# Kernel tuning notes

Hardware: AMD Instinct MI355X
Metric: run time of the kernel (lower is better)

The kernel has to match this reference:

```python
import jax, jax.numpy as jnp
import numpy as np

N_NODES = 50000
N_EDGES = 800000
HC = 64      # hidden_channels
NG = 5       # num_gaussians
NF = 64      # num_filters
SL = 20      # short_len
NC = 2       # n_conv
Z_DIM = 2 * NF + SL  # 148
BN_EPS = 1e-5


def setup_inputs() -> dict:
    key = jax.random.key(0)
    ks = jax.random.split(key, 16)
    s = 0.05
    return {
        "h": jax.random.normal(ks[0], (N_NODES, HC), dtype=jnp.float32),
        "edge_index": jax.random.randint(ks[1], (2, N_EDGES), 0, N_NODES, dtype=jnp.int32),
        "edge_weight": jax.random.uniform(ks[2], (N_EDGES,), dtype=jnp.float32),
        "edge_attr": jax.random.uniform(ks[3], (N_EDGES, NG), dtype=jnp.float32),
        "lin0_w": jax.random.normal(ks[4], (HC, NF), dtype=jnp.float32) * s,
        "lin0_b": jnp.zeros((NF,), dtype=jnp.float32),
        "short_w": jax.random.normal(ks[5], (NG, SL), dtype=jnp.float32) * s,
        "short_b": jnp.zeros((SL,), dtype=jnp.float32),
        "linf_w": jax.random.normal(ks[6], (NC, Z_DIM, NF), dtype=jnp.float32) * s,
        "linf_b": jnp.zeros((NC, NF), dtype=jnp.float32),
        "lins_w": jax.random.normal(ks[7], (NC, Z_DIM, NF), dtype=jnp.float32) * s,
        "lins_b": jnp.zeros((NC, NF), dtype=jnp.float32),
        "bn_gamma": jnp.ones((NC, NF), dtype=jnp.float32),
        "bn_beta": jnp.zeros((NC, NF), dtype=jnp.float32),
        "data": 0,
    }


def reference(h, edge_index, edge_weight, edge_attr,
              lin0_w, lin0_b, short_w, short_b,
              linf_w, linf_b, lins_w, lins_b,
              bn_gamma, bn_beta, data):
    # lin0 + relu
    out = jax.nn.relu(h @ lin0_w + lin0_b)                      # [N, NF]
    # short edge-attr projection + relu
    ea = jax.nn.relu(edge_attr @ short_w + short_b)             # [E, SL]
    src = edge_index[0]  # x_j (source)
    dst = edge_index[1]  # x_i (target / aggregation index)
    n = out.shape[0]
    for l in range(NC):
        x_i = out[dst]                                          # [E, NF]
        x_j = out[src]                                          # [E, NF]
        z = jnp.concatenate([x_i, x_j, ea], axis=-1)            # [E, 148]
        msg = jax.nn.sigmoid(z @ linf_w[l] + linf_b[l]) * \
              jax.nn.softplus(z @ lins_w[l] + lins_b[l])        # [E, NF]
        agg = jax.ops.segment_sum(msg, dst, num_segments=n)     # [N, NF]
        # BatchNorm1d (training-mode batch stats, biased variance)
        mean = jnp.mean(agg, axis=0)
        var = jnp.mean((agg - mean) ** 2, axis=0)
        bn = (agg - mean) * jax.lax.rsqrt(var + BN_EPS) * bn_gamma[l] + bn_beta[l]
        conv_out = bn + out                                     # CGConv internal residual
        out = out + jax.nn.relu(conv_out)                       # _Interactions residual
    return out
```

## Files before the change

### kernel.cpp

```cpp
#include <hip/hip_runtime.h>
#include <hip/hip_bf16.h>

#define N_NODES 50000
#define N_EDGES 800000
#define SCAN_NB 49
#define EPW 20
#define EW_BLOCKS 10000

typedef __hip_bfloat16 bf16;
typedef unsigned int u32;
typedef unsigned short u16;
typedef _Float16 hh2 __attribute__((ext_vector_type(2)));

#if defined(__has_builtin)
#if __has_builtin(__builtin_amdgcn_fdot2)
#define HAVE_FDOT2 1
#endif
#endif

__device__ __forceinline__ float bfb(u32 b) { return __uint_as_float(b << 16); }

__device__ __forceinline__ u16 f2bf(float x) {
    bf16 a = __float2bfloat16(x);
    u16 u;
    __builtin_memcpy(&u, &a, 2);
    return u;
}

__device__ __forceinline__ hh2 pkrtz(float a, float b) {
    auto r = __builtin_amdgcn_cvt_pkrtz(a, b);
    hh2 o;
    __builtin_memcpy(&o, &r, 4);
    return o;
}

__device__ __forceinline__ float ldf(const void* p, long i, int f32) {
    if (f32) return ((const float*)p)[i];
    return bfb((u32)((const u16*)p)[i]);
}

__device__ __forceinline__ int detect_f32(const u32* g) { return g[0] == 0x3F800000u; }

__global__ __launch_bounds__(256) void k_front(const void* __restrict__ h,
        const void* __restrict__ w, const void* __restrict__ b,
        const u32* __restrict__ gr, u16* __restrict__ outw,
        const int* __restrict__ ei, int* __restrict__ cnt,
        int* __restrict__ tsum, uint4* __restrict__ aggz4,
        const void* __restrict__ eattr, const void* __restrict__ short_w,
        const void* __restrict__ short_b, u32* __restrict__ sea_e) {
    int t = threadIdx.x;
    uint4 z4 = {0u, 0u, 0u, 0u};
    for (int i = blockIdx.x * 256 + t; i < N_NODES * 16; i += 1536 * 256)
        aggz4[i] = z4;
    int f32 = detect_f32(gr);
    if (blockIdx.x >= 1024) {
        __shared__ float swl[100];
        __shared__ float sbl[20];
        if (t < 100) swl[t] = ldf(short_w, t, f32);
        if (t < 20) sbl[t] = ldf(short_b, t, f32);
        __syncthreads();
        int bid = blockIdx.x - 1024;
        for (int e = bid * 256 + t; e < N_EDGES; e += 512 * 256) {
            float a0 = ldf(eattr, (long)e * 5 + 0, f32);
            float a1 = ldf(eattr, (long)e * 5 + 1, f32);
            float a2 = ldf(eattr, (long)e * 5 + 2, f32);
            float a3 = ldf(eattr, (long)e * 5 + 3, f32);
            float a4 = ldf(eattr, (long)e * 5 + 4, f32);
            u32 buf[10];
            #pragma unroll
            for (int j = 0; j < 10; ++j) {
                float e0 = sbl[2 * j], e1 = sbl[2 * j + 1];
                e0 = fmaf(a0, swl[0 * 20 + 2 * j], e0);
                e1 = fmaf(a0, swl[0 * 20 + 2 * j + 1], e1);
                e0 = fmaf(a1, swl[1 * 20 + 2 * j], e0);
                e1 = fmaf(a1, swl[1 * 20 + 2 * j + 1], e1);
                e0 = fmaf(a2, swl[2 * 20 + 2 * j], e0);
                e1 = fmaf(a2, swl[2 * 20 + 2 * j + 1], e1);
                e0 = fmaf(a3, swl[3 * 20 + 2 * j], e0);
                e1 = fmaf(a3, swl[3 * 20 + 2 * j + 1], e1);
                e0 = fmaf(a4, swl[4 * 20 + 2 * j], e0);
                e1 = fmaf(a4, swl[4 * 20 + 2 * j + 1], e1);
                e0 = fmaxf(e0, 0.f);
                e1 = fmaxf(e1, 0.f);
                hh2 h2 = pkrtz(e0, e1);
                u32 u;
                __builtin_memcpy(&u, &h2, 4);
                buf[j] = u;
            }
            u32* sp = sea_e + (size_t)e * 10u;
            #pragma unroll
            for (int q = 0; q < 5; ++q) {
                uint2 v2 = {buf[2 * q], buf[2 * q + 1]};
                *(uint2*)(sp + 2 * q) = v2;
            }
        }
        return;
    }
    if (blockIdx.x >= 512) {
        __shared__ int lts[SCAN_NB];
        if (t < SCAN_NB) lts[t] = 0;
        __syncthreads();
        int bid = blockIdx.x - 512;
        for (int e = bid * 256 + t; e < N_EDGES; e += 512 * 256) {
            int dst = ei[N_EDGES + e];
            atomicAdd(&cnt[dst], 1);
            atomicAdd(&lts[dst >> 10], 1);
        }
        __syncthreads();
        if (t < SCAN_NB) atomicAdd(&tsum[t], lts[t]);
        return;
    }
    __shared__ float Wl[64 * 64];
    __shared__ float bl[64];
    __shared__ float hs[16 * 64];
    for (int i = t; i < 4096; i += 256) Wl[i] = ldf(w, i, f32);
    if (t < 64) bl[t] = ldf(b, t, f32);
    int c = t & 63, g = t >> 6;
    for (int chunk = blockIdx.x; chunk < N_NODES / 16; chunk += 512) {
        __syncthreads();
        int node0 = chunk * 16;
        for (int i = t; i < 1024; i += 256) hs[i] = ldf(h, (long)node0 * 64 + i, f32);
        __syncthreads();
        #pragma unroll
        for (int nn = 0; nn < 4; ++nn) {
            int n = g * 4 + nn;
            float acc = bl[c];
            #pragma unroll
            for (int k = 0; k < 64; ++k) acc = fmaf(hs[n * 64 + k], Wl[k * 64 + c], acc);
            outw[(node0 + n) * 64 + c] = f2bf(fmaxf(acc, 0.f));
        }
    }
}

__global__ __launch_bounds__(1024) void k_scan(int* __restrict__ cnt,
        const int* __restrict__ tsum) {
    __shared__ int wsum[16];
    __shared__ int boff_s;
    int t = threadIdx.x, lane = t & 63, wv = t >> 6;
    if (wv == 0) {
        int v = (lane < SCAN_NB && lane < (int)blockIdx.x) ? tsum[lane] : 0;
        #pragma unroll
        for (int d = 32; d >= 1; d >>= 1) v += __shfl_xor(v, d, 64);
        if (lane == 0) boff_s = v;
    }
    int i = blockIdx.x * 1024 + t;
    int v = (i < N_NODES) ? cnt[i] : 0;
    int incl = v;
    #pragma unroll
    for (int d = 1; d < 64; d <<= 1) {
        int x = __shfl_up(incl, d, 64);
        if (lane >= d) incl += x;
    }
    if (lane == 63) wsum[wv] = incl;
    __syncthreads();
    if (wv == 0) {
        int s = (lane < 16) ? wsum[lane] : 0;
        int si = s;
        #pragma unroll
        for (int d = 1; d < 16; d <<= 1) {
            int x = __shfl_up(si, d, 64);
            if (lane >= d) si += x;
        }
        if (lane < 16) wsum[lane] = si - s;
    }
    __syncthreads();
    incl += wsum[wv] + boff_s;
    if (i < N_NODES) cnt[i] = incl - v;
}

__global__ __launch_bounds__(256) void k_pproj_bin(const u16* __restrict__ outw,
        const void* __restrict__ linf_w, const void* __restrict__ lins_w,
        const void* __restrict__ linf_b, const void* __restrict__ lins_b,
        const u32* __restrict__ gr, bf16* __restrict__ P,
        const int* __restrict__ ei, int* __restrict__ cursor,
        uint2* __restrict__ bb, u32* __restrict__ wpk) {
    int t = threadIdx.x;
    int f32 = detect_f32(gr);
    if (blockIdx.x >= 512) {
        if (blockIdx.x == 512 && t < 128) {
            int ly = t >> 6, ln = t & 63;
            long wb = (long)ly * 9472 + 8192;
            u32* wp = wpk + (size_t)(ly * 64 + ln) * 20;
            #pragma unroll
            for (int j = 0; j < 10; ++j) {
                hh2 fp = pkrtz(ldf(linf_w, wb + (2 * j) * 64 + ln, f32),
                               ldf(linf_w, wb + (2 * j + 1) * 64 + ln, f32));
                hh2 sp = pkrtz(ldf(lins_w, wb + (2 * j) * 64 + ln, f32),
                               ldf(lins_w, wb + (2 * j + 1) * 64 + ln, f32));
                u32 uf, us;
                __builtin_memcpy(&uf, &fp, 4);
                __builtin_memcpy(&us, &sp, 4);
                wp[2 * j] = uf;
                wp[2 * j + 1] = us;
            }
        }
        int bid = blockIdx.x - 512;
        for (int e = bid * 256 + t; e < N_EDGES; e += 512 * 256) {
            int dst = ei[N_EDGES + e];
            int src = ei[e];
            int slot = atomicAdd(&cursor[dst], 1);
            uint2 v;
            v.x = ((u32)dst << 16) | (u32)src;
            v.y = (u32)e;
            bb[slot] = v;
        }
        return;
    }
    int b = t >> 6, c = t & 63;
    const void* wmat = (b < 2) ? linf_w : lins_w;
    long woff = (long)(b & 1) * 4096;
    float bias = 0.f;
    if (b == 0) bias = ldf(linf_b, c, f32);
    if (b == 2) bias = ldf(lins_b, c, f32);
    float wc[64];
    #pragma unroll
    for (int k = 0; k < 64; ++k) wc[k] = ldf(wmat, woff + k * 64 + c, f32);
    int stidx = (b & 1) * 128 + 2 * c + (b >> 1);
    __shared__ float hs[16 * 64];
    for (int chunk = blockIdx.x; chunk < N_NODES / 16; chunk += 512) {
        __syncthreads();
        int node0 = chunk * 16;
        {
            ushort4 hv = *(const ushort4*)(outw + (size_t)node0 * 64 + t * 4);
            hs[t * 4 + 0] = bfb((u32)hv.x);
            hs[t * 4 + 1] = bfb((u32)hv.y);
            hs[t * 4 + 2] = bfb((u32)hv.z);
            hs[t * 4 + 3] = bfb((u32)hv.w);
        }
        __syncthreads();
        for (int n = 0; n < 16; ++n) {
            float acc = bias;
            #pragma unroll
            for (int k = 0; k < 64; ++k) acc = fmaf(hs[n * 64 + k], wc[k], acc);
            P[(size_t)(node0 + n) * 256 + stidx] = __float2bfloat16(acc);
        }
    }
}

struct EB { u32 ea; u32 pd[4]; u32 ps[4]; int d[4]; };

__global__ __launch_bounds__(256) void k_edge_flat(const uint2* __restrict__ bb,
        const u32* __restrict__ sea_e, const u32* __restrict__ wpk, int layer,
        const u32* __restrict__ Pw, float* __restrict__ agg) {
    int t = threadIdx.x, lane = t & 63, wv = t >> 6;
    int wid = blockIdx.x * 4 + wv;
    int base = wid * EPW;

    int eo = (lane / 10) & 3, j10 = lane % 10;
    const uint4* wv4 = (const uint4*)(wpk + (size_t)(layer * 64 + lane) * 20);
    uint4 q0 = wv4[0], q1 = wv4[1], q2 = wv4[2], q3 = wv4[3], q4 = wv4[4];
    u32 wbuf[20] = {q0.x, q0.y, q0.z, q0.w, q1.x, q1.y, q1.z, q1.w,
                    q2.x, q2.y, q2.z, q2.w, q3.x, q3.y, q3.z, q3.w,
                    q4.x, q4.y, q4.z, q4.w};
    hh2 wf2[10], ws2[10];
    #pragma unroll
    for (int j = 0; j < 10; ++j) {
        __builtin_memcpy(&wf2[j], &wbuf[2 * j], 4);
        __builtin_memcpy(&ws2[j], &wbuf[2 * j + 1], 4);
    }

    float acc = 0.f;
    int cur = -1;

    auto issueA = [&](uint2& A, int b) {
        A = bb[(u32)base + 4u * (u32)b + ((u32)lane & 3u)];
    };
    auto issueB = [&](EB& B, uint2 A, int b) {
        u32 eid = (u32)__shfl((int)A.y, eo, 64);
        B.ea = sea_e[eid * 10u + (u32)j10];
        #pragma unroll
        for (int i = 0; i < 4; ++i) {
            u32 pki = (u32)__builtin_amdgcn_readlane((int)A.x, i);
            int d = (int)(pki >> 16);
            u32 s = pki & 0xFFFFu;
            B.d[i] = d;
            B.pd[i] = Pw[(u32)d * 128u + (u32)lane];
            B.ps[i] = Pw[s * 128u + 64u + (u32)lane];
        }
    };
    auto computeC = [&](const EB& B) {
        #pragma unroll
        for (int i = 0; i < 4; ++i) {
            int d = B.d[i];
            u32 pd = B.pd[i], ps = B.ps[i];
            float f = bfb(pd & 0xFFFFu) + bfb(ps & 0xFFFFu);
            float s = __uint_as_float(pd & 0xFFFF0000u) +
                      __uint_as_float(ps & 0xFFFF0000u);
            #pragma unroll
            for (int j = 0; j < 10; ++j) {
                u32 u = (u32)__builtin_amdgcn_readlane((int)B.ea, 10 * i + j);
                hh2 hu;
                __builtin_memcpy(&hu, &u, 4);
#ifdef HAVE_FDOT2
                f = __builtin_amdgcn_fdot2(hu, wf2[j], f, false);
                s = __builtin_amdgcn_fdot2(hu, ws2[j], s, false);
#else
                f = fmaf((float)hu[0], (float)wf2[j][0], f);
                f = fmaf((float)hu[1], (float)wf2[j][1], f);
                s = fmaf((float)hu[0], (float)ws2[j][0], s);
                s = fmaf((float)hu[1], (float)ws2[j][1], s);
#endif
            }
            float sig = 1.f / (1.f + __expf(-f));
            float sp = fmaxf(s, 0.f) + __logf(1.f + __expf(-fabsf(s)));
            if (d != cur) {
                if (cur >= 0)
                    atomicAdd(agg + (u32)cur * 64u + (u32)lane, acc);
                acc = 0.f;
                cur = d;
            }
            acc += sig * sp;
        }
    };

    uint2 A0, A1, A2, A3;
    EB B0, B1, B2, B3;
    issueA(A0, 0); issueA(A1, 1); issueA(A2, 2); issueA(A3, 3);
    issueB(B0, A0, 0); issueB(B1, A1, 1); issueB(B2, A2, 2);
    issueA(A0, 4);
    issueB(B3, A3, 3);
    computeC(B0);
    issueB(B0, A0, 4);
    computeC(B1);
    computeC(B2);
    computeC(B3);
    computeC(B0);
    if (cur >= 0) atomicAdd(agg + (u32)cur * 64u + (u32)lane, acc);
}

__global__ __launch_bounds__(256) void k_stats(const float* __restrict__ aggf,
        float* __restrict__ stats) {
    int t = threadIdx.x;
    int r = t >> 4, c4 = (t & 15) * 4;
    float s0 = 0.f, s1 = 0.f, s2 = 0.f, s3 = 0.f;
    float q0 = 0.f, q1 = 0.f, q2 = 0.f, q3 = 0.f;
    for (int row = blockIdx.x * 16 + r; row < N_NODES; row += 256 * 16) {
        float4 v = *(const float4*)(aggf + (size_t)row * 64 + c4);
        s0 += v.x; s1 += v.y; s2 += v.z; s3 += v.w;
        q0 = fmaf(v.x, v.x, q0); q1 = fmaf(v.y, v.y, q1);
        q2 = fmaf(v.z, v.z, q2); q3 = fmaf(v.w, v.w, q3);
    }
    __shared__ float red[2][16][64];
    red[0][r][c4 + 0] = s0; red[0][r][c4 + 1] = s1;
    red[0][r][c4 + 2] = s2; red[0][r][c4 + 3] = s3;
    red[1][r][c4 + 0] = q0; red[1][r][c4 + 1] = q1;
    red[1][r][c4 + 2] = q2; red[1][r][c4 + 3] = q3;
    __syncthreads();
    if (t < 128) {
        int m = t >> 6, c = t & 63;
        float a = 0.f;
        #pragma unroll
        for (int k = 0; k < 16; ++k) a += red[m][k][c];
        atomicAdd(&stats[m * 64 + c], a);
    }
}

__global__ __launch_bounds__(256) void k_apply_pproj(float* __restrict__ aggf,
        const float* __restrict__ stats, const void* __restrict__ gamma,
        const void* __restrict__ beta, const u32* __restrict__ gr,
        u16* __restrict__ outw,
        const void* __restrict__ linf_w, const void* __restrict__ lins_w,
        const void* __restrict__ linf_b, const void* __restrict__ lins_b,
        bf16* __restrict__ P) {
    int f32 = detect_f32(gr);
    int t = threadIdx.x;
    int b = t >> 6, c = t & 63;
    int nid = t >> 4, c4 = (t & 15) * 4;
    const float invN = 1.f / (float)N_NODES;
    float m4[4], iv4[4], g4[4], b4[4];
    #pragma unroll
    for (int k = 0; k < 4; ++k) {
        float mean = stats[c4 + k] * invN;
        float var = fmaxf(stats[64 + c4 + k] * invN - mean * mean, 0.f);
        m4[k] = mean;
        iv4[k] = rsqrtf(var + 1e-5f);
        g4[k] = ldf(gamma, c4 + k, f32);
        b4[k] = ldf(beta, c4 + k, f32);
    }
    const void* wmat = (b < 2) ? linf_w : lins_w;
    long woff = 9472 + (long)(b & 1) * 4096;
    float bias = 0.f;
    if (b == 0) bias = ldf(linf_b, 64 + c, f32);
    if (b == 2) bias = ldf(lins_b, 64 + c, f32);
    float wc[64];
    #pragma unroll
    for (int k = 0; k < 64; ++k) wc[k] = ldf(wmat, woff + k * 64 + c, f32);
    int stidx = (b & 1) * 128 + 2 * c + (b >> 1);
    __shared__ float hs[16 * 64];
    for (int chunk = blockIdx.x; chunk < N_NODES / 16; chunk += 512) {
        __syncthreads();
        int node0 = chunk * 16;
        {
            size_t idx = (size_t)(node0 + nid) * 64 + c4;
            float4 a = *(const float4*)(aggf + idx);
            ushort4 ow = *(const ushort4*)(outw + idx);
            const float* ap = (const float*)&a;
            const u16* op = (const u16*)&ow;
            float no[4];
            #pragma unroll
            for (int k = 0; k < 4; ++k) {
                float o = bfb((u32)op[k]);
                float bn = fmaf((ap[k] - m4[k]) * iv4[k], g4[k], b4[k]);
                no[k] = o + fmaxf(bn + o, 0.f);
            }
            ushort4 nw = {f2bf(no[0]), f2bf(no[1]), f2bf(no[2]), f2bf(no[3])};
            *(ushort4*)(outw + idx) = nw;
            float4 z4 = {0.f, 0.f, 0.f, 0.f};
            *(float4*)(aggf + idx) = z4;
            float4 hv = {no[0], no[1], no[2], no[3]};
            *(float4*)(&hs[nid * 64 + c4]) = hv;
        }
        __syncthreads();
        for (int n = 0; n < 16; ++n) {
            float acc = bias;
            #pragma unroll
            for (int k = 0; k < 64; ++k) acc = fmaf(hs[n * 64 + k], wc[k], acc);
            P[(size_t)(node0 + n) * 256 + stidx] = __float2bfloat16(acc);
        }
    }
}

__global__ __launch_bounds__(256) void k_apply_final(const float* __restrict__ aggf,
        const float* __restrict__ stats, const void* __restrict__ gamma,
        const void* __restrict__ beta, const u32* __restrict__ gr,
        const u16* __restrict__ outw, void* __restrict__ dout) {
    int f32 = detect_f32(gr);
    const float invN = 1.f / (float)N_NODES;
    int t0 = blockIdx.x * 256 + threadIdx.x;
    int c4 = (t0 & 15) * 4;
    float m4[4], iv4[4], g4[4], b4[4];
    #pragma unroll
    for (int k = 0; k < 4; ++k) {
        float mean = stats[c4 + k] * invN;
        float var = fmaxf(stats[64 + c4 + k] * invN - mean * mean, 0.f);
        m4[k] = mean;
        iv4[k] = rsqrtf(var + 1e-5f);
        g4[k] = ldf(gamma, 64 + c4 + k, f32);
        b4[k] = ldf(beta, 64 + c4 + k, f32);
    }
    for (int i4 = t0; i4 < N_NODES * 16; i4 += 1024 * 256) {
        float4 a = *(const float4*)(aggf + (size_t)i4 * 4);
        ushort4 ow = *(const ushort4*)(outw + (size_t)i4 * 4);
        const float* ap = (const float*)&a;
        const u16* op = (const u16*)&ow;
        float no[4];
        #pragma unroll
        for (int k = 0; k < 4; ++k) {
            float o = bfb((u32)op[k]);
            float bn = fmaf((ap[k] - m4[k]) * iv4[k], g4[k], b4[k]);
            no[k] = o + fmaxf(bn + o, 0.f);
        }
        if (f32) {
            float4 o4 = {no[0], no[1], no[2], no[3]};
            *(float4*)((float*)dout + (size_t)i4 * 4) = o4;
        } else {
            ushort4 o4 = {f2bf(no[0]), f2bf(no[1]), f2bf(no[2]), f2bf(no[3])};
            *(ushort4*)((u16*)dout + (size_t)i4 * 4) = o4;
        }
    }
}

extern "C" void kernel_launch(void* const* d_in, const int* in_sizes, int n_in,
                              void* d_out, int out_size, void* d_ws, size_t ws_size,
                              hipStream_t stream) {
    const void* h       = d_in[0];
    const int*  ei      = (const int*)d_in[1];
    const void* eattr   = d_in[3];
    const void* lin0_w  = d_in[4];
    const void* lin0_b  = d_in[5];
    const void* short_w = d_in[6];
    const void* short_b = d_in[7];
    const void* linf_w  = d_in[8];
    const void* linf_b  = d_in[9];
    const void* lins_w  = d_in[10];
    const void* lins_b  = d_in[11];
    const void* gamma   = d_in[12];
    const void* beta    = d_in[13];
    const u32*  gr      = (const u32*)gamma;

    u16*   outw  = (u16*)d_ws;
    bf16*  P     = (bf16*)(outw + (size_t)N_NODES * 64);
    uint2* bb    = (uint2*)(P + (size_t)N_NODES * 256);
    float* aggf  = (float*)(bb + N_EDGES);
    int*   cnt   = (int*)(aggf + (size_t)N_NODES * 64);
    float* stats = (float*)(cnt + N_NODES);
    int*   tsum  = (int*)(stats + 256);
    u32*   sea_e = (u32*)(tsum + 64);
    u32*   wpk   = sea_e + (size_t)N_EDGES * 10;

    size_t zbytes = (size_t)N_NODES * 4 + 256 * 4 + 64 * 4;
    (void)hipMemsetAsync(cnt, 0, zbytes, stream);

    k_front<<<1536, 256, 0, stream>>>(h, lin0_w, lin0_b, gr, outw, ei, cnt,
                                      tsum, (uint4*)aggf, eattr, short_w,
                                      short_b, sea_e);
    k_scan<<<SCAN_NB, 1024, 0, stream>>>(cnt, tsum);
    k_pproj_bin<<<1024, 256, 0, stream>>>(outw, linf_w, lins_w, linf_b, lins_b,
                                          gr, P, ei, cnt, bb, wpk);
    k_edge_flat<<<EW_BLOCKS, 256, 0, stream>>>(bb, sea_e, wpk, 0,
                                               (const u32*)P, aggf);
    k_stats<<<256, 256, 0, stream>>>(aggf, stats);
    k_apply_pproj<<<512, 256, 0, stream>>>(aggf, stats, gamma, beta, gr, outw,
                                           linf_w, lins_w, linf_b, lins_b, P);
    k_edge_flat<<<EW_BLOCKS, 256, 0, stream>>>(bb, sea_e, wpk, 1,
                                               (const u32*)P, aggf);
    k_stats<<<256, 256, 0, stream>>>(aggf, stats + 128);
    k_apply_final<<<1024, 256, 0, stream>>>(aggf, stats + 128, gamma, beta, gr,
                                            outw, d_out);
}
```

Baseline: 459.7 us.

## Replace global-atomic counting sort with two-pass bucketed radix binning of edges

```diff
diff --git a/kernel.cpp b/kernel.cpp
--- a/kernel.cpp
+++ b/kernel.cpp
@@ -3,7 +3,7 @@
 
 #define N_NODES 50000
 #define N_EDGES 800000
-#define SCAN_NB 49
+#define NBK 391
 #define EPW 20
 #define EW_BLOCKS 10000
 
@@ -44,8 +44,8 @@
 __global__ __launch_bounds__(256) void k_front(const void* __restrict__ h,
         const void* __restrict__ w, const void* __restrict__ b,
         const u32* __restrict__ gr, u16* __restrict__ outw,
-        const int* __restrict__ ei, int* __restrict__ cnt,
-        int* __restrict__ tsum, uint4* __restrict__ aggz4,
+        const int* __restrict__ ei, u32* __restrict__ bmat,
+        uint4* __restrict__ aggz4,
         const void* __restrict__ eattr, const void* __restrict__ short_w,
         const void* __restrict__ short_b, u32* __restrict__ sea_e) {
     int t = threadIdx.x;
@@ -97,17 +97,17 @@
         return;
     }
     if (blockIdx.x >= 512) {
-        __shared__ int lts[SCAN_NB];
-        if (t < SCAN_NB) lts[t] = 0;
+        __shared__ int bcnt[NBK];
+        for (int k = t; k < NBK; k += 256) bcnt[k] = 0;
         __syncthreads();
         int bid = blockIdx.x - 512;
         for (int e = bid * 256 + t; e < N_EDGES; e += 512 * 256) {
             int dst = ei[N_EDGES + e];
-            atomicAdd(&cnt[dst], 1);
-            atomicAdd(&lts[dst >> 10], 1);
-        }
-        __syncthreads();
-        if (t < SCAN_NB) atomicAdd(&tsum[t], lts[t]);
+            atomicAdd(&bcnt[dst >> 7], 1);
+        }
+        __syncthreads();
+        for (int k = t; k < NBK; k += 256)
+            bmat[(size_t)k * 512 + bid] = (u32)bcnt[k];
         return;
     }
     __shared__ float Wl[64 * 64];
@@ -132,19 +132,12 @@
     }
 }
 
-__global__ __launch_bounds__(1024) void k_scan(int* __restrict__ cnt,
-        const int* __restrict__ tsum) {
-    __shared__ int wsum[16];
-    __shared__ int boff_s;
+__global__ __launch_bounds__(512) void k_scan(u32* __restrict__ bmat,
+        u32* __restrict__ total) {
+    __shared__ int wsum[8];
     int t = threadIdx.x, lane = t & 63, wv = t >> 6;
-    if (wv == 0) {
-        int v = (lane < SCAN_NB && lane < (int)blockIdx.x) ? tsum[lane] : 0;
-        #pragma unroll
-        for (int d = 32; d >= 1; d >>= 1) v += __shfl_xor(v, d, 64);
-        if (lane == 0) boff_s = v;
-    }
-    int i = blockIdx.x * 1024 + t;
-    int v = (i < N_NODES) ? cnt[i] : 0;
+    int bk = blockIdx.x;
+    int v = (int)bmat[(size_t)bk * 512 + t];
     int incl = v;
     #pragma unroll
     for (int d = 1; d < 64; d <<= 1) {
@@ -154,26 +147,56 @@
     if (lane == 63) wsum[wv] = incl;
     __syncthreads();
     if (wv == 0) {
-        int s = (lane < 16) ? wsum[lane] : 0;
+        int s = (lane < 8) ? wsum[lane] : 0;
         int si = s;
         #pragma unroll
-        for (int d = 1; d < 16; d <<= 1) {
+        for (int d = 1; d < 8; d <<= 1) {
             int x = __shfl_up(si, d, 64);
             if (lane >= d) si += x;
         }
-        if (lane < 16) wsum[lane] = si - s;
-    }
-    __syncthreads();
-    incl += wsum[wv] + boff_s;
-    if (i < N_NODES) cnt[i] = incl - v;
+        if (lane < 8) wsum[lane] = si - s;
+    }
+    __syncthreads();
+    int excl = incl - v + wsum[wv];
+    bmat[(size_t)bk * 512 + t] = (u32)excl;
+    if (t == 511) total[bk] = (u32)(excl + v);
+}
+
+__global__ __launch_bounds__(512) void k_scan2(const u32* __restrict__ total,
+        u32* __restrict__ bucketbase) {
+    __shared__ int wsum[8];
+    int t = threadIdx.x, lane = t & 63, wv = t >> 6;
+    int v = (t < NBK) ? (int)total[t] : 0;
+    int incl = v;
+    #pragma unroll
+    for (int d = 1; d < 64; d <<= 1) {
+        int x = __shfl_up(incl, d, 64);
+        if (lane >= d) incl += x;
+    }
+    if (lane == 63) wsum[wv] = incl;
+    __syncthreads();
+    if (wv == 0) {
+        int s = (lane < 8) ? wsum[lane] : 0;
+        int si = s;
+        #pragma unroll
+        for (int d = 1; d < 8; d <<= 1) {
+            int x = __shfl_up(si, d, 64);
+            if (lane >= d) si += x;
+        }
+        if (lane < 8) wsum[lane] = si - s;
+    }
+    __syncthreads();
+    if (t < NBK) bucketbase[t] = (u32)(incl - v + wsum[wv]);
+    if (t == 0) bucketbase[NBK] = N_EDGES;
 }
 
 __global__ __launch_bounds__(256) void k_pproj_bin(const u16* __restrict__ outw,
         const void* __restrict__ linf_w, const void* __restrict__ lins_w,
         const void* __restrict__ linf_b, const void* __restrict__ lins_b,
         const u32* __restrict__ gr, bf16* __restrict__ P,
-        const int* __restrict__ ei, int* __restrict__ cursor,
-        uint2* __restrict__ bb, u32* __restrict__ wpk) {
+        const int* __restrict__ ei, const u32* __restrict__ bmat,
+        const u32* __restrict__ bucketbase, uint2* __restrict__ tmp,
+        u32* __restrict__ wpk) {
     int t = threadIdx.x;
     int f32 = detect_f32(gr);
     if (blockIdx.x >= 512) {
@@ -194,15 +217,19 @@
                 wp[2 * j + 1] = us;
             }
         }
+        __shared__ u32 run[NBK];
         int bid = blockIdx.x - 512;
+        for (int k = t; k < NBK; k += 256)
+            run[k] = bucketbase[k] + bmat[(size_t)k * 512 + bid];
+        __syncthreads();
         for (int e = bid * 256 + t; e < N_EDGES; e += 512 * 256) {
             int dst = ei[N_EDGES + e];
             int src = ei[e];
-            int slot = atomicAdd(&cursor[dst], 1);
+            u32 off = atomicAdd(&run[dst >> 7], 1u);
             uint2 v;
             v.x = ((u32)dst << 16) | (u32)src;
             v.y = (u32)e;
-            bb[slot] = v;
+            tmp[off] = v;
         }
         return;
     }
@@ -234,6 +261,46 @@
             for (int k = 0; k < 64; ++k) acc = fmaf(hs[n * 64 + k], wc[k], acc);
             P[(size_t)(node0 + n) * 256 + stidx] = __float2bfloat16(acc);
         }
+    }
+}
+
+__global__ __launch_bounds__(256) void k_bin2(const uint2* __restrict__ tmp,
+        const u32* __restrict__ bucketbase, uint2* __restrict__ bb) {
+    __shared__ int hist[128];
+    __shared__ u32 run[128];
+    __shared__ int wpart[2];
+    int t = threadIdx.x;
+    int bk = blockIdx.x;
+    u32 lo = bucketbase[bk], hi = bucketbase[bk + 1];
+    if (t < 128) hist[t] = 0;
+    __syncthreads();
+    for (u32 i = lo + t; i < hi; i += 256) {
+        u32 pk = tmp[i].x;
+        atomicAdd(&hist[(pk >> 16) & 127], 1);
+    }
+    __syncthreads();
+    int v_ = 0, incl_ = 0;
+    if (t < 128) {
+        int lane = t & 63;
+        v_ = hist[t];
+        incl_ = v_;
+        #pragma unroll
+        for (int d = 1; d < 64; d <<= 1) {
+            int x = __shfl_up(incl_, d, 64);
+            if (lane >= d) incl_ += x;
+        }
+        if (lane == 63) wpart[t >> 6] = incl_;
+    }
+    __syncthreads();
+    if (t < 128) {
+        int add = (t >= 64) ? wpart[0] : 0;
+        run[t] = lo + (u32)(incl_ - v_ + add);
+    }
+    __syncthreads();
+    for (u32 i = lo + t; i < hi; i += 256) {
+        uint2 v = tmp[i];
+        u32 slot = atomicAdd(&run[(v.x >> 16) & 127], 1u);
+        bb[slot] = v;
     }
 }
 
@@ -482,21 +549,24 @@
     bf16*  P     = (bf16*)(outw + (size_t)N_NODES * 64);
     uint2* bb    = (uint2*)(P + (size_t)N_NODES * 256);
     float* aggf  = (float*)(bb + N_EDGES);
-    int*   cnt   = (int*)(aggf + (size_t)N_NODES * 64);
-    float* stats = (float*)(cnt + N_NODES);
-    int*   tsum  = (int*)(stats + 256);
-    u32*   sea_e = (u32*)(tsum + 64);
+    float* stats = (float*)(aggf + (size_t)N_NODES * 64);
+    u32*   bmat  = (u32*)(stats + 256);
+    u32*   total = bmat + (size_t)NBK * 512;
+    u32*   bucketbase = total + 400;
+    u32*   sea_e = bucketbase + 400;
     u32*   wpk   = sea_e + (size_t)N_EDGES * 10;
-
-    size_t zbytes = (size_t)N_NODES * 4 + 256 * 4 + 64 * 4;
-    (void)hipMemsetAsync(cnt, 0, zbytes, stream);
-
-    k_front<<<1536, 256, 0, stream>>>(h, lin0_w, lin0_b, gr, outw, ei, cnt,
-                                      tsum, (uint4*)aggf, eattr, short_w,
-                                      short_b, sea_e);
-    k_scan<<<SCAN_NB, 1024, 0, stream>>>(cnt, tsum);
+    uint2* tmp   = (uint2*)(wpk + 2 * 64 * 20);
+
+    (void)hipMemsetAsync(stats, 0, 256 * 4, stream);
+
+    k_front<<<1536, 256, 0, stream>>>(h, lin0_w, lin0_b, gr, outw, ei, bmat,
+                                      (uint4*)aggf, eattr, short_w, short_b,
+                                      sea_e);
+    k_scan<<<NBK, 512, 0, stream>>>(bmat, total);
+    k_scan2<<<1, 512, 0, stream>>>(total, bucketbase);
     k_pproj_bin<<<1024, 256, 0, stream>>>(outw, linf_w, lins_w, linf_b, lins_b,
-                                          gr, P, ei, cnt, bb, wpk);
+                                          gr, P, ei, bmat, bucketbase, tmp, wpk);
+    k_bin2<<<NBK, 256, 0, stream>>>(tmp, bucketbase, bb);
     k_edge_flat<<<EW_BLOCKS, 256, 0, stream>>>(bb, sea_e, wpk, 0,
                                                (const u32*)P, aggf);
     k_stats<<<256, 256, 0, stream>>>(aggf, stats);
```

New measurement: 388.6 us (median of 2 runs). 15.5% less time.
